# Kernel tuning notes

Measured on AMD Instinct MI355X. Metric: run time of the kernel, lower is better.

## Reference

```python
import jax, jax.numpy as jnp
import numpy as np

CONF = 0.3      # confidence threshold (NMS.conf)
IOU = 0.6       # IoU threshold (NMS.iou)
MAX_WH = 4096.0 # class-offset trick for per-class NMS
K = 2048        # max candidates entering NMS (yolov5-style cap)
MAX_DET = 300   # max detections kept per image (fixed output size)


def setup_inputs() -> dict:
    key = jax.random.key(0)
    kxy, kwh, kobj, kcls = jax.random.split(key, 4)
    B, N, NC = 8, 25200, 80
    # realistic raw predictions: xywh in pixel units for a 640x640 image
    xy = jax.random.uniform(kxy, (B, N, 2), minval=0.0, maxval=640.0)
    wh = jax.random.uniform(kwh, (B, N, 2), minval=2.0, maxval=160.0)
    obj = jax.random.uniform(kobj, (B, N, 1))
    cls = jax.random.uniform(kcls, (B, N, NC))
    x = jnp.concatenate([xy, wh, obj, cls], axis=-1)  # [B, N, 5+NC]
    return {"x": x}


def _xywh2xyxy(b):
    xy, half = b[..., :2], b[..., 2:4] * 0.5
    return jnp.concatenate([xy - half, xy + half], axis=-1)


def _pairwise_iou(boxes):  # boxes: [K, 4] xyxy -> [K, K]
    lt = jnp.maximum(boxes[:, None, :2], boxes[None, :, :2])
    rb = jnp.minimum(boxes[:, None, 2:], boxes[None, :, 2:])
    inter = jnp.clip(rb - lt, 0.0).prod(-1)
    area = (boxes[:, 2] - boxes[:, 0]) * (boxes[:, 3] - boxes[:, 1])
    return inter / (area[:, None] + area[None, :] - inter + 1e-9)


def _nms_single(pred):  # pred: [N, 5+NC]
    obj = pred[:, 4]
    cls_conf = pred[:, 5:] * obj[:, None]          # conf = obj * cls prob
    conf = cls_conf.max(-1)
    cls_id = jnp.argmax(cls_conf, -1)
    valid = (obj > CONF) & (conf > CONF)           # candidate + final threshold
    boxes = _xywh2xyxy(pred[:, :4])
    scores = jnp.where(valid, conf, -1.0)
    top_s, idx = jax.lax.top_k(scores, K)          # cap candidates, sorted desc
    boxes_k = boxes[idx]
    cls_k = cls_id[idx]
    valid_k = top_s > 0.0
    # offset boxes by class so NMS is per-class
    shifted = boxes_k + cls_k[:, None].astype(boxes_k.dtype) * MAX_WH
    iou = _pairwise_iou(shifted)                   # [K, K]
    order = jnp.arange(K)

    def body(keep, i):  # greedy suppression in score order
        active = keep[i] & valid_k[i]
        sup = (iou[i] > IOU) & (order > i)
        keep = jnp.where(active, keep & ~sup, keep)
        return keep, None

    keep, _ = jax.lax.scan(body, jnp.ones((K,), bool), order)
    keep = keep & valid_k
    final_s = jnp.where(keep, top_s, -1.0)
    det_s, det_i = jax.lax.top_k(final_s, MAX_DET)
    dets = jnp.concatenate(
        [boxes_k[det_i], top_s[det_i][:, None],
         cls_k[det_i][:, None].astype(boxes_k.dtype)], axis=-1)  # [MAX_DET, 6]
    return dets, det_s > 0.0


def reference(x):
    # returns (dets [B, MAX_DET, 6] = xyxy,conf,cls ; valid mask [B, MAX_DET])
    return jax.vmap(_nms_single)(x)
```

## Files before the change

kernel.cpp:

```cpp
#include <hip/hip_runtime.h>
#include <hip/hip_bf16.h>

#define B 8
#define N 25200
#define ROW 85
#define NC 80
#define K 2048
#define MAXDET 300
#define NBUCKET 16384
#define CAND_CAP 4096
#define NCHUNK 32
#define STILE 64

__global__ void __launch_bounds__(256)
nms_score_kernel(const float* __restrict__ x,
                 float* __restrict__ scores,
                 int* __restrict__ cls_id) {
    int b = blockIdx.y;
    int i0 = blockIdx.x * STILE;
    int rows = N - i0; if (rows > STILE) rows = STILE;
    __shared__ float lx[STILE * ROW];
    {
        const float4* s4 = (const float4*)(x + ((size_t)b * N + i0) * ROW);
        float4* d4 = (float4*)lx;
        int nv = rows * ROW / 4;
        for (int k = threadIdx.x; k < nv; k += 256) d4[k] = s4[k];
    }
    __syncthreads();
    int g = threadIdx.x >> 2;
    int q = threadIdx.x & 3;
    if (g >= rows) return;
    const float* p = lx + g * ROW;
    float obj = p[4];
    float best = -1e30f;
    int bc = 127;
    if (obj > 0.3f) {
        #pragma unroll
        for (int k = 0; k < 20; ++k) {
            int c = q + 4 * k;
            float v = __fmul_rn(p[5 + c], obj);
            if (v > best) { best = v; bc = c; }
        }
    }
    #pragma unroll
    for (int m = 1; m < 4; m <<= 1) {
        float ov = __shfl_xor(best, m, 64);
        int   oc = __shfl_xor(bc, m, 64);
        if (ov > best || (ov == best && oc < bc)) { best = ov; bc = oc; }
    }
    if (q == 0) {
        int i = i0 + g;
        float score = (obj > 0.3f && best > 0.3f) ? best : -1.0f;
        scores[b * N + i] = score;
        cls_id[b * N + i] = (bc == 127) ? 0 : bc;
    }
}

__global__ void __launch_bounds__(1024, 1)
nms_select_kernel(const float* __restrict__ scores,
                  const float* __restrict__ x,
                  const int* __restrict__ cls_id,
                  float* __restrict__ top_s,
                  float* __restrict__ boxes,
                  int* __restrict__ clsk,
                  float* __restrict__ shifted,
                  float* __restrict__ area) {
    __shared__ unsigned loff[NBUCKET];
    __shared__ unsigned lcnt16[NBUCKET / 2];
    __shared__ unsigned long long lk[CAND_CAP];
    __shared__ unsigned wsum[16];

    int b = blockIdx.x;
    int t = threadIdx.x;
    int ln = t & 63, wv = t >> 6;
    constexpr int NITER = (N + 1023) / 1024;

    {
        uint4 z = {0u, 0u, 0u, 0u};
        uint4* d1 = (uint4*)loff;
        for (int k = t; k < NBUCKET / 4; k += 1024) d1[k] = z;
        uint4* d2 = (uint4*)lcnt16;
        for (int k = t; k < NBUCKET / 8; k += 1024) d2[k] = z;
    }
    for (int k = t; k < CAND_CAP; k += 1024) lk[k] = 0ULL;
    __syncthreads();

    float sreg[NITER];
    #pragma unroll
    for (int r = 0; r < NITER; ++r) {
        int i = t + r * 1024;
        float s = (i < N) ? scores[b * N + i] : -1.0f;
        sreg[r] = s;
        if (s > 0.0f) {
            int q = (int)(__fmul_rn(s, 16384.0f));
            if (q > NBUCKET - 1) q = NBUCKET - 1;
            atomicAdd(&loff[q], 1u);
        }
    }
    __syncthreads();

    unsigned v[16];
    int base_j = t * 16;
    unsigned A4 = (unsigned)(NBUCKET - 16 - base_j) / 4;
    {
        uint4 u0 = ((uint4*)loff)[A4 + 0];
        uint4 u1 = ((uint4*)loff)[A4 + 1];
        uint4 u2 = ((uint4*)loff)[A4 + 2];
        uint4 u3 = ((uint4*)loff)[A4 + 3];
        unsigned u[16] = {u0.x,u0.y,u0.z,u0.w, u1.x,u1.y,u1.z,u1.w,
                          u2.x,u2.y,u2.z,u2.w, u3.x,u3.y,u3.z,u3.w};
        #pragma unroll
        for (int k = 0; k < 16; ++k) v[k] = u[15 - k];
    }
    unsigned S = 0;
    #pragma unroll
    for (int k = 0; k < 16; ++k) S += v[k];
    unsigned pref = S;
    #pragma unroll
    for (int o = 1; o < 64; o <<= 1) { unsigned u = __shfl_up(pref, o, 64); if (ln >= o) pref += u; }
    if (ln == 63) wsum[wv] = pref;
    __syncthreads();
    unsigned wbase = 0;
    for (int w = 0; w < wv; ++w) wbase += wsum[w];
    unsigned running = wbase + pref - S;
    {
        unsigned o[16];
        #pragma unroll
        for (int k = 0; k < 16; ++k) { o[15 - k] = running; running += v[k]; }
        ((uint4*)loff)[A4 + 0] = make_uint4(o[0],  o[1],  o[2],  o[3]);
        ((uint4*)loff)[A4 + 1] = make_uint4(o[4],  o[5],  o[6],  o[7]);
        ((uint4*)loff)[A4 + 2] = make_uint4(o[8],  o[9],  o[10], o[11]);
        ((uint4*)loff)[A4 + 3] = make_uint4(o[12], o[13], o[14], o[15]);
    }
    __syncthreads();

    #pragma unroll
    for (int r = 0; r < NITER; ++r) {
        float s = sreg[r];
        if (s > 0.0f) {
            int i = t + r * 1024;
            int q = (int)(__fmul_rn(s, 16384.0f));
            if (q > NBUCKET - 1) q = NBUCKET - 1;
            unsigned start = loff[q];
            if (start < CAND_CAP) {
                unsigned sh = (q & 1) * 16;
                unsigned old = atomicAdd(&lcnt16[q >> 1], 1u << sh);
                unsigned rank = (old >> sh) & 0xFFFFu;
                unsigned pos = start + rank;
                if (pos < CAND_CAP) {
                    unsigned long long key =
                        ((unsigned long long)__float_as_uint(s) << 32) | (unsigned)(~i);
                    lk[pos] = key;
                }
            }
        }
    }
    __syncthreads();

    for (int q = t; q < NBUCKET; q += 1024) {
        unsigned start = loff[q];
        if (start < CAND_CAP) {
            unsigned c = (lcnt16[q >> 1] >> ((q & 1) * 16)) & 0xFFFFu;
            unsigned m = c;
            if (m > CAND_CAP - start) m = CAND_CAP - start;
            if (m >= 2) {
                for (unsigned a = start + 1; a < start + m; ++a) {
                    unsigned long long kv = lk[a];
                    unsigned p2 = a;
                    while (p2 > start && lk[p2 - 1] < kv) { lk[p2] = lk[p2 - 1]; --p2; }
                    lk[p2] = kv;
                }
            }
        }
    }
    __syncthreads();

    for (int r = t; r < K; r += 1024) {
        unsigned long long key = lk[r];
        float s;
        int idx;
        float x1, y1, x2, y2;
        int c;
        if (key == 0ULL) {
            s = -1.0f; x1 = y1 = x2 = y2 = 0.0f; c = 0;
        } else {
            s = __uint_as_float((unsigned)(key >> 32));
            idx = (int)(~(unsigned)key);
            const float* p = x + ((size_t)b * N + idx) * ROW;
            float cx = p[0], cy = p[1], w = p[2], h = p[3];
            float hx = __fmul_rn(w, 0.5f);
            float hy = __fmul_rn(h, 0.5f);
            x1 = __fsub_rn(cx, hx); y1 = __fsub_rn(cy, hy);
            x2 = __fadd_rn(cx, hx); y2 = __fadd_rn(cy, hy);
            c = cls_id[b * N + idx];
        }
        int o = b * K + r;
        top_s[o] = s;
        boxes[o * 4 + 0] = x1; boxes[o * 4 + 1] = y1;
        boxes[o * 4 + 2] = x2; boxes[o * 4 + 3] = y2;
        clsk[o] = c;
        float sh = __fmul_rn((float)c, 4096.0f);
        float sx1 = __fadd_rn(x1, sh), sy1 = __fadd_rn(y1, sh);
        float sx2 = __fadd_rn(x2, sh), sy2 = __fadd_rn(y2, sh);
        shifted[o * 4 + 0] = sx1; shifted[o * 4 + 1] = sy1;
        shifted[o * 4 + 2] = sx2; shifted[o * 4 + 3] = sy2;
        area[o] = __fmul_rn(__fsub_rn(sx2, sx1), __fsub_rn(sy2, sy1));
    }
}

__global__ void nms_mask_kernel(const float* __restrict__ shifted,
                                const float* __restrict__ area,
                                unsigned long long* __restrict__ maskT,
                                unsigned long long* __restrict__ nzT) {
    int L = blockIdx.x, b = blockIdx.y;
    int jb = (int)((__fsqrt_rn(8.0f * (float)L + 1.0f) - 1.0f) * 0.5f);
    while ((jb + 1) * (jb + 2) / 2 <= L) ++jb;
    while (jb * (jb + 1) / 2 > L) --jb;
    int ib = L - jb * (jb + 1) / 2;
    int t = threadIdx.x;
    int i = ib * 64 + t;

    __shared__ float jbox[64][4];
    __shared__ float jarea[64];
    int j0 = jb * 64;
    {
        const float* sb = shifted + ((size_t)b * K + j0 + t) * 4;
        jbox[t][0] = sb[0]; jbox[t][1] = sb[1]; jbox[t][2] = sb[2]; jbox[t][3] = sb[3];
        jarea[t] = area[b * K + j0 + t];
    }
    __syncthreads();

    const float* ab = shifted + ((size_t)b * K + i) * 4;
    float ax1 = ab[0], ay1 = ab[1], ax2 = ab[2], ay2 = ab[3];
    float aarea = area[b * K + i];

    unsigned long long mycol = 0ULL;
    for (int jl = 0; jl < 64; ++jl) {
        int j = j0 + jl;
        bool cond = false;
        if (j > i) {
            float lx = fmaxf(ax1, jbox[jl][0]);
            float ly = fmaxf(ay1, jbox[jl][1]);
            float rx = fminf(ax2, jbox[jl][2]);
            float ry = fminf(ay2, jbox[jl][3]);
            float w = fmaxf(__fsub_rn(rx, lx), 0.0f);
            float h = fmaxf(__fsub_rn(ry, ly), 0.0f);
            float inter = __fmul_rn(w, h);
            float denom = __fadd_rn(__fsub_rn(__fadd_rn(aarea, jarea[jl]), inter), 1e-9f);
            float iou = __fdiv_rn(inter, denom);
            cond = iou > 0.6f;
        }
        unsigned long long colm = __ballot(cond);
        if (t == jl) mycol = colm;
    }
    maskT[((size_t)b * K + j0 + t) * NCHUNK + ib] = mycol;
    unsigned long long nzb = __ballot(mycol != 0ULL);
    if (t == 0) nzT[((size_t)b * NCHUNK + jb) * NCHUNK + ib] = nzb;
}

__global__ void __launch_bounds__(1024)
nms_reduce_out_kernel(const unsigned long long* __restrict__ maskT,
                      const unsigned long long* __restrict__ nzT,
                      const float* __restrict__ top_s,
                      const float* __restrict__ boxes,
                      const int* __restrict__ clsk,
                      float* __restrict__ out) {
    int b = blockIdx.x;
    int t = threadIdx.x;
    int ln = t & 63, wv = t >> 6;
    __shared__ unsigned long long kept[NCHUNK], decided[NCHUNK];
    __shared__ unsigned long long snapk[NCHUNK], snapd[NCHUNK];
    __shared__ int nundec;
    if (t == 0) nundec = 0;
    __syncthreads();

    int st[2];
    #pragma unroll
    for (int h = 0; h < 2; ++h) {
        int c = wv + h * 16;
        int j = c * 64 + ln;
        unsigned long long w = (ln < NCHUNK)
            ? nzT[((size_t)b * NCHUNK + c) * NCHUNK + ln] : 0ULL;
        #pragma unroll
        for (int m = 1; m < 64; m <<= 1) w |= __shfl_xor(w, m, 64);
        bool valid = top_s[b * K + j] > 0.0f;
        bool hassup = ((w >> ln) & 1ULL) != 0ULL;
        bool k_local = valid && !hassup;
        bool d_local = !valid || !hassup;
        st[h] = d_local ? 1 : 0;
        unsigned long long kb = __ballot(k_local);
        unsigned long long db = __ballot(d_local);
        if (ln == 0) {
            kept[c] = kb;
            decided[c] = db;
            if (~db != 0ULL) atomicAdd(&nundec, __popcll(~db));
        }
    }

    for (int round = 0; round < 2048; ++round) {
        __syncthreads();
        if (nundec == 0) break;
        if (t < NCHUNK) { snapd[t] = decided[t]; snapk[t] = kept[t]; }
        __syncthreads();
        #pragma unroll
        for (int h = 0; h < 2; ++h) {
            if (st[h]) continue;
            int j = t + h * 1024;
            const unsigned long long* row = maskT + ((size_t)b * K + j) * NCHUNK;
            int nw = (j >> 6) + 1;
            unsigned long long pend = 0ULL, sup = 0ULL;
            for (int w = 0; w < nw; ++w) {
                unsigned long long r = row[w];
                pend |= r & ~snapd[w];
                sup  |= r & snapk[w];
            }
            if (pend == 0ULL) {
                unsigned long long bit = 1ULL << (j & 63);
                if (sup == 0ULL) atomicOr(&kept[j >> 6], bit);
                atomicOr(&decided[j >> 6], bit);
                st[h] = 1;
                atomicSub(&nundec, 1);
            }
        }
    }
    __syncthreads();

    if (wv == 0) {
        int lane = ln;
        int total = 0;
        for (int c = 0; c < NCHUNK; ++c) {
            bool k = ((kept[c] >> lane) & 1ULL) != 0ULL;
            unsigned long long m = __ballot(k);
            total += __popcll(m);
        }
        float* dets  = out + (size_t)b * MAXDET * 6;
        float* flags = out + (size_t)B * MAXDET * 6 + (size_t)b * MAXDET;
        unsigned long long below = (lane == 0) ? 0ULL : (~0ULL >> (64 - lane));
        int kc = 0, nc = 0;
        for (int c = 0; c < NCHUNK; ++c) {
            int i = c * 64 + lane;
            bool k = ((kept[c] >> lane) & 1ULL) != 0ULL;
            unsigned long long m = __ballot(k);
            int pc = __popcll(m);
            int slot = k ? (kc + __popcll(m & below))
                         : (total + nc + __popcll((~m) & below));
            if (slot < MAXDET) {
                int o = b * K + i;
                dets[slot * 6 + 0] = boxes[o * 4 + 0];
                dets[slot * 6 + 1] = boxes[o * 4 + 1];
                dets[slot * 6 + 2] = boxes[o * 4 + 2];
                dets[slot * 6 + 3] = boxes[o * 4 + 3];
                dets[slot * 6 + 4] = top_s[o];
                dets[slot * 6 + 5] = (float)clsk[o];
                flags[slot] = k ? 1.0f : 0.0f;
            }
            kc += pc;
            nc += 64 - pc;
        }
    }
}

extern "C" void kernel_launch(void* const* d_in, const int* in_sizes, int n_in,
                              void* d_out, int out_size, void* d_ws, size_t ws_size,
                              hipStream_t stream) {
    const float* x = (const float*)d_in[0];
    float* out = (float*)d_out;

    char* ws = (char*)d_ws;
    size_t off = 0;
    auto alloc = [&](size_t bytes) -> void* {
        void* p = ws + off;
        off += bytes;
        off = (off + 255) & ~(size_t)255;
        return p;
    };

    float*    scores = (float*)    alloc((size_t)B * N * 4);
    int*      cls_id = (int*)      alloc((size_t)B * N * 4);
    float*    top_s  = (float*)    alloc((size_t)B * K * 4);
    float*    boxes  = (float*)    alloc((size_t)B * K * 4 * 4);
    int*      clsk   = (int*)      alloc((size_t)B * K * 4);
    float*    shifted= (float*)    alloc((size_t)B * K * 4 * 4);
    float*    area   = (float*)    alloc((size_t)B * K * 4);
    unsigned long long* maskT = (unsigned long long*) alloc((size_t)B * K * NCHUNK * 8);
    unsigned long long* nzT   = (unsigned long long*) alloc((size_t)B * NCHUNK * NCHUNK * 8);
    (void)ws_size;

    nms_score_kernel<<<dim3((N + STILE - 1) / STILE, B), 256, 0, stream>>>(x, scores, cls_id);
    nms_select_kernel<<<B, 1024, 0, stream>>>(scores, x, cls_id,
                                              top_s, boxes, clsk, shifted, area);
    nms_mask_kernel<<<dim3(NCHUNK * (NCHUNK + 1) / 2, B), 64, 0, stream>>>(shifted, area, maskT, nzT);
    nms_reduce_out_kernel<<<B, 1024, 0, stream>>>(maskT, nzT, top_s, boxes, clsk, out);
}
```

Measured before the change: 161.0 us.

## Build score histogram in parallel score kernel via global atomics

Measured after the change: 166.5 us. 3.5% more time.

```diff
diff --git a/kernel.cpp b/kernel.cpp
--- a/kernel.cpp
+++ b/kernel.cpp
@@ -15,7 +15,8 @@
 __global__ void __launch_bounds__(256)
 nms_score_kernel(const float* __restrict__ x,
                  float* __restrict__ scores,
-                 int* __restrict__ cls_id) {
+                 int* __restrict__ cls_id,
+                 unsigned* __restrict__ hist) {
     int b = blockIdx.y;
     int i0 = blockIdx.x * STILE;
     int rows = N - i0; if (rows > STILE) rows = STILE;
@@ -50,14 +51,20 @@
     }
     if (q == 0) {
         int i = i0 + g;
-        float score = (obj > 0.3f && best > 0.3f) ? best : -1.0f;
-        scores[b * N + i] = score;
+        bool valid = (obj > 0.3f && best > 0.3f);
+        scores[b * N + i] = valid ? best : -1.0f;
         cls_id[b * N + i] = (bc == 127) ? 0 : bc;
+        if (valid) {
+            int qq = (int)(__fmul_rn(best, 16384.0f));
+            if (qq > NBUCKET - 1) qq = NBUCKET - 1;
+            atomicAdd(&hist[b * NBUCKET + qq], 1u);
+        }
     }
 }
 
 __global__ void __launch_bounds__(1024, 1)
-nms_select_kernel(const float* __restrict__ scores,
+nms_select_kernel(const unsigned* __restrict__ hist,
+                  const float* __restrict__ scores,
                   const float* __restrict__ x,
                   const int* __restrict__ cls_id,
                   float* __restrict__ top_s,
@@ -73,30 +80,16 @@
     int b = blockIdx.x;
     int t = threadIdx.x;
     int ln = t & 63, wv = t >> 6;
-    constexpr int NITER = (N + 1023) / 1024;
-
-    {
+
+    {
+        const uint4* src = (const uint4*)(hist + b * NBUCKET);
+        uint4* d1 = (uint4*)loff;
+        for (int k = t; k < NBUCKET / 4; k += 1024) d1[k] = src[k];
         uint4 z = {0u, 0u, 0u, 0u};
-        uint4* d1 = (uint4*)loff;
-        for (int k = t; k < NBUCKET / 4; k += 1024) d1[k] = z;
         uint4* d2 = (uint4*)lcnt16;
         for (int k = t; k < NBUCKET / 8; k += 1024) d2[k] = z;
     }
     for (int k = t; k < CAND_CAP; k += 1024) lk[k] = 0ULL;
-    __syncthreads();
-
-    float sreg[NITER];
-    #pragma unroll
-    for (int r = 0; r < NITER; ++r) {
-        int i = t + r * 1024;
-        float s = (i < N) ? scores[b * N + i] : -1.0f;
-        sreg[r] = s;
-        if (s > 0.0f) {
-            int q = (int)(__fmul_rn(s, 16384.0f));
-            if (q > NBUCKET - 1) q = NBUCKET - 1;
-            atomicAdd(&loff[q], 1u);
-        }
-    }
     __syncthreads();
 
     unsigned v[16];
@@ -134,11 +127,9 @@
     }
     __syncthreads();
 
-    #pragma unroll
-    for (int r = 0; r < NITER; ++r) {
-        float s = sreg[r];
+    for (int i = t; i < N; i += 1024) {
+        float s = scores[b * N + i];
         if (s > 0.0f) {
-            int i = t + r * 1024;
             int q = (int)(__fmul_rn(s, 16384.0f));
             if (q > NBUCKET - 1) q = NBUCKET - 1;
             unsigned start = loff[q];
@@ -377,6 +368,7 @@
 
     float*    scores = (float*)    alloc((size_t)B * N * 4);
     int*      cls_id = (int*)      alloc((size_t)B * N * 4);
+    unsigned* hist   = (unsigned*) alloc((size_t)B * NBUCKET * 4);
     float*    top_s  = (float*)    alloc((size_t)B * K * 4);
     float*    boxes  = (float*)    alloc((size_t)B * K * 4 * 4);
     int*      clsk   = (int*)      alloc((size_t)B * K * 4);
@@ -386,8 +378,9 @@
     unsigned long long* nzT   = (unsigned long long*) alloc((size_t)B * NCHUNK * NCHUNK * 8);
     (void)ws_size;
 
-    nms_score_kernel<<<dim3((N + STILE - 1) / STILE, B), 256, 0, stream>>>(x, scores, cls_id);
-    nms_select_kernel<<<B, 1024, 0, stream>>>(scores, x, cls_id,
+    hipMemsetAsync(hist, 0, (size_t)B * NBUCKET * 4, stream);
+    nms_score_kernel<<<dim3((N + STILE - 1) / STILE, B), 256, 0, stream>>>(x, scores, cls_id, hist);
+    nms_select_kernel<<<B, 1024, 0, stream>>>(hist, scores, x, cls_id,
                                               top_s, boxes, clsk, shifted, area);
     nms_mask_kernel<<<dim3(NCHUNK * (NCHUNK + 1) / 2, B), 64, 0, stream>>>(shifted, area, maskT, nzT);
     nms_reduce_out_kernel<<<B, 1024, 0, stream>>>(maskT, nzT, top_s, boxes, clsk, out);
```
